# Optimization experiments

Hardware: AMD Instinct MI355X
Metric: run time of the kernel (lower is better)

Reference implementation:

```python
import jax, jax.numpy as jnp
import numpy as np

N_IN, N_LAT, LEN_T, N_SHIFT = 128, 21, 51, 50
N_HID, BATCH = 4, 2048


def identity_init(n_rows, n_cols):
    A = np.zeros((n_rows, n_cols), np.float32)
    if n_rows >= n_cols:
        k = n_rows - n_cols + 1
        for c in range(n_cols):
            A[c:c + k, c] = 1.0 / k
    else:
        k = n_cols - n_rows + 1
        for r in range(n_rows):
            A[r, r:r + k] = 1.0 / k
    return jnp.asarray(A)


def setup_inputs() -> dict:
    key = jax.random.key(0)
    ks = jax.random.split(key, 8)
    s = 0.05
    return {
        'inputs': jax.random.normal(ks[0], (BATCH, LEN_T, N_IN), dtype=jnp.float32),
        'enc_W': jax.random.normal(ks[1], (N_HID, N_IN, N_IN), dtype=jnp.float32) * s,
        'enc_b': jnp.zeros((N_HID, N_IN), jnp.float32),
        'enc_Wout': jax.random.normal(ks[2], (N_IN, N_IN), dtype=jnp.float32) * s,
        'enc_bout': jnp.zeros((N_IN,), jnp.float32),
        'dec_W': jax.random.normal(ks[3], (N_HID, N_IN, N_IN), dtype=jnp.float32) * s,
        'dec_b': jnp.zeros((N_HID, N_IN), jnp.float32),
        'dec_Wout': jax.random.normal(ks[4], (N_IN, N_IN), dtype=jnp.float32) * s,
        'dec_bout': jnp.zeros((N_IN,), jnp.float32),
        'W_enc_inner': identity_init(N_IN, N_LAT),
        'L': jnp.eye(N_LAT, dtype=jnp.float32),
        'W_dec_inner': identity_init(N_LAT, N_IN),
    }


def res_block(x, Ws, bs, Wout, bout):
    # DenseResBlock: ReLU hidden dense stack + linear output + identity skip
    h = x
    for i in range(Ws.shape[0]):
        h = jax.nn.relu(h @ Ws[i] + bs[i])
    return h @ Wout + bout + x


def reference(inputs, enc_W, enc_b, enc_Wout, enc_bout,
              dec_W, dec_b, dec_Wout, dec_bout,
              W_enc_inner, L, W_dec_inner):
    B = inputs.shape[0]
    len_pred = LEN_T - N_SHIFT  # = 1

    # ---- autoencoder branch (all timesteps flattened into rows) ----
    auto_in = inputs.reshape(-1, N_IN)                       # [B*T, n_in]
    part_enc = res_block(auto_in, enc_W, enc_b, enc_Wout, enc_bout)
    full_enc = part_enc @ W_enc_inner                        # [B*T, n_lat]
    part_dec = full_enc @ W_dec_inner                        # [B*T, n_in]
    autoencoder_output = res_block(part_dec, dec_W, dec_b, dec_Wout, dec_bout)
    autoencoder_output = autoencoder_output.reshape(B, LEN_T, N_IN)
    outer_auto_output = res_block(part_enc, dec_W, dec_b, dec_Wout, dec_bout)
    outer_auto_output = outer_auto_output.reshape(B, LEN_T, N_IN)

    # ---- prediction branch: recurrent application of Koopman operator L ----
    pred_in = inputs[:, :len_pred, :].reshape(-1, N_IN)      # [B*len_pred, n_in]
    cur = res_block(pred_in, enc_W, enc_b, enc_Wout, enc_bout) @ W_enc_inner

    def step(cur_enc, _):
        adv = cur_enc @ L                                    # [B*len_pred, n_lat]
        dec = res_block(adv @ W_dec_inner, dec_W, dec_b, dec_Wout, dec_bout)
        return adv, dec

    _, preds = jax.lax.scan(step, cur, None, length=N_SHIFT)  # [S, B*lp, n_in]
    preds = preds.reshape(N_SHIFT, B, len_pred, N_IN)
    predictions = preds.transpose(1, 0, 2, 3).reshape(B, N_SHIFT * len_pred, N_IN)

    return autoencoder_output, outer_auto_output, predictions
```

## Files before the change

kernel.cpp:

```cpp
#include <hip/hip_runtime.h>
#include <stdint.h>


typedef _Float16 h8 __attribute__((ext_vector_type(8)));
typedef _Float16 h4 __attribute__((ext_vector_type(4)));
typedef float    f4 __attribute__((ext_vector_type(4)));

#define ROWS_AUTO 104448
#define NT64      1632
#define NUNITS    2432

#define WT_ENCW      0
#define WT_ENCWOUT   (4*16384)
#define WT_DECW      (5*16384)
#define WT_DECWOUT   (9*16384)
#define WT_COMB      (10*16384)

#define MFULL_OFF_B 0x60000
#define ACH_OFF_B   0x200000
#define PE_OFF_B    0x220000
#define PET0_OFF_B  0x1C00000

#define H0 0
#define H1 16384
#define H2 32768
#define H3 49152
#define LDSE (49152 + 2560)
#define LDSD (65536 + 2560)

#define hsw(rl, c) ((rl)*256 + ((((c)) ^ ((rl) & 7)) << 4))

#define PIN(B) asm volatile("" : "+v"(B[0]), "+v"(B[1]), "+v"(B[2]), "+v"(B[3]), \
                                 "+v"(B[4]), "+v"(B[5]), "+v"(B[6]), "+v"(B[7]))

__device__ __forceinline__ f4 mfma16(h8 a, h8 b, f4 c) {
  return __builtin_amdgcn_mfma_f32_16x16x32_f16(a, b, c, 0, 0, 0);
}
__device__ __forceinline__ h8 cvt8(f4 a, f4 b) {
  h8 r;
  r[0]=(_Float16)a[0]; r[1]=(_Float16)a[1]; r[2]=(_Float16)a[2]; r[3]=(_Float16)a[3];
  r[4]=(_Float16)b[0]; r[5]=(_Float16)b[1]; r[6]=(_Float16)b[2]; r[7]=(_Float16)b[3];
  return r;
}
__device__ __forceinline__ void loadW(h8 B[8], const _Float16* gW, int nbase, int r15, int hi) {
#pragma unroll
  for (int nt = 0; nt < 2; ++nt)
#pragma unroll
    for (int ks = 0; ks < 4; ++ks)
      B[nt*4+ks] = *(const h8*)(gW + (size_t)(nbase + nt*16 + r15)*128 + ks*32 + hi*8);
}

__device__ __forceinline__ void mmF4s(const char* sm, int hb, const h8 B[8],
                                      f4 acc[4][2], int r15, int hi) {
#pragma unroll
  for (int rt = 0; rt < 4; ++rt) { acc[rt][0] = (f4){0,0,0,0}; acc[rt][1] = (f4){0,0,0,0}; }
#pragma unroll
  for (int ks = 0; ks < 4; ++ks) {
    int c = ks*4 + hi;
    h8 a[4];
#pragma unroll
    for (int rt = 0; rt < 4; ++rt) a[rt] = *(const h8*)(sm + hb + hsw(rt*16 + r15, c));
#pragma unroll
    for (int rt = 0; rt < 4; ++rt) {
      acc[rt][0] = mfma16(B[ks],   a[rt], acc[rt][0]);
      acc[rt][1] = mfma16(B[4+ks], a[rt], acc[rt][1]);
    }
  }
}

__device__ __forceinline__ void hw4s(char* sm, int hb, int wbase, const f4 acc[4][2],
                                     const float* bl, int bo, int r15, int hi) {
  f4 bb0 = *(const f4*)(bl + bo + wbase + hi*4);
  f4 bb1 = *(const f4*)(bl + bo + wbase + 16 + hi*4);
  int bo2 = (hi & 1) * 8;
#pragma unroll
  for (int nt = 0; nt < 2; ++nt) {
    int c = ((wbase + nt*16) >> 3) + (hi >> 1);
    f4 bb = nt ? bb1 : bb0;
#pragma unroll
    for (int rt = 0; rt < 4; ++rt) {
      int row = rt*16 + r15;
      h4 p;
#pragma unroll
      for (int d = 0; d < 4; ++d) p[d] = (_Float16)fmaxf(acc[rt][nt][d] + bb[d], 0.f);
      *(h4*)(sm + hb + row*256 + ((c ^ (row & 7)) << 4) + bo2) = p;
    }
  }
}
__device__ __forceinline__ void hw4r(char* sm, int hb, int wbase, const f4 acc[4][2],
                                     int r15, int hi) {
  int bo2 = (hi & 1) * 8;
#pragma unroll
  for (int nt = 0; nt < 2; ++nt) {
    int c = ((wbase + nt*16) >> 3) + (hi >> 1);
#pragma unroll
    for (int rt = 0; rt < 4; ++rt) {
      int row = rt*16 + r15;
      h4 p;
#pragma unroll
      for (int d = 0; d < 4; ++d) p[d] = (_Float16)acc[rt][nt][d];
      *(h4*)(sm + hb + row*256 + ((c ^ (row & 7)) << 4) + bo2) = p;
    }
  }
}

__device__ __forceinline__ void epi_direct(const char* sm, int hskip, int wbase,
                                           const f4 acc[4][2], const float* bl,
                                           float* dst, int rstride, int r15, int hi) {
  f4 bb0 = *(const f4*)(bl + 512 + wbase + hi*4);
  f4 bb1 = *(const f4*)(bl + 512 + wbase + 16 + hi*4);
  int bo2 = (hi & 1) * 8;
#pragma unroll
  for (int nt = 0; nt < 2; ++nt) {
    int c = ((wbase + nt*16) >> 3) + (hi >> 1);
    int n0 = wbase + nt*16 + hi*4;
    f4 bb = nt ? bb1 : bb0;
#pragma unroll
    for (int rt = 0; rt < 4; ++rt) {
      int row = rt*16 + r15;
      h4 sk = *(const h4*)(sm + hskip + row*256 + ((c ^ (row & 7)) << 4) + bo2);
      f4 v;
#pragma unroll
      for (int d = 0; d < 4; ++d) v[d] = acc[rt][nt][d] + bb[d] + (float)sk[d];
      *(f4*)(dst + (size_t)row*rstride + n0) = v;
    }
  }
}

#define LAYD(HIN, HOUT, BW, BO) do {                                 \
    mmF4s(sm, HIN, BW, acc, r15, hi);                                \
    hw4s(sm, HOUT, wbase, acc, bl, BO, r15, hi);                     \
    __syncthreads();                                                 \
  } while (0)


__global__ __launch_bounds__(512) void k_prep(
    const float* __restrict__ encW, const float* __restrict__ encWout,
    const float* __restrict__ decW, const float* __restrict__ decWout,
    const float* __restrict__ L,
    _Float16* __restrict__ wt, float* __restrict__ ach) {
  __shared__ float chA[441], chB[441];
  int m = blockIdx.y, tid = threadIdx.x;
  if (m == 10) {
    if (blockIdx.x != 0) return;
    if (tid < 441) chA[tid] = L[tid];
    __syncthreads();
    for (int s = 0; s < 50; ++s) {
      if (tid < 441) ach[s*441 + tid] = chA[tid];
      if (s == 49) break;
      if (tid < 441) {
        int i = tid / 21, j = tid % 21; float a = 0.f;
        for (int k = 0; k < 21; ++k) a += chA[i*21 + k] * L[k*21 + j];
        chB[tid] = a;
      }
      __syncthreads();
      if (tid < 441) chA[tid] = chB[tid];
      __syncthreads();
    }
    return;
  }
  int idx = blockIdx.x*512 + tid;
  if (idx >= 16384) return;
  const float* src; _Float16* dst;
  if (m < 4)       { src = encW + m*16384;     dst = wt + WT_ENCW + m*16384; }
  else if (m == 4) { src = encWout;            dst = wt + WT_ENCWOUT; }
  else if (m < 9)  { src = decW + (m-5)*16384; dst = wt + WT_DECW + (m-5)*16384; }
  else             { src = decWout;            dst = wt + WT_DECWOUT; }
  int n = idx >> 7, k = idx & 127;
  dst[idx] = (_Float16)src[k*128 + n];
}

__global__ __launch_bounds__(512) void k_aux(
    const float* __restrict__ ach, const float* __restrict__ wencI,
    const float* __restrict__ wdecI,
    _Float16* __restrict__ mfull, _Float16* __restrict__ wt) {
  __shared__ float T1[2688];
  __shared__ float sa[441];
  int s = blockIdx.x, t = threadIdx.x;
  if (s < 50) {
    if (t < 441) sa[t] = ach[s*441 + t];
    __syncthreads();
    for (int idx = t; idx < 2688; idx += 512) {
      int k = idx / 21, j = idx % 21;
      float a = 0.f;
      for (int u = 0; u < 21; ++u) a += wencI[k*21 + u] * sa[u*21 + j];
      T1[idx] = a;
    }
  } else {
    for (int idx = t; idx < 2688; idx += 512) T1[idx] = wencI[idx];
  }
  __syncthreads();
  _Float16* dst = (s < 50) ? (mfull + (size_t)s*16384) : (wt + WT_COMB);
  for (int idx = t; idx < 16384; idx += 512) {
    int n = idx >> 7, k = idx & 127;
    float a = 0.f;
    for (int j = 0; j < 21; ++j) a += T1[k*21 + j] * wdecI[j*128 + n];
    dst[idx] = (_Float16)a;
  }
}


__global__ __launch_bounds__(256, 2) void k_enc(
    const float* __restrict__ x, const _Float16* __restrict__ wt,
    const float* __restrict__ enc_b, const float* __restrict__ enc_bout,
    _Float16* __restrict__ pe_ws, _Float16* __restrict__ pet0) {
  __shared__ char sm[LDSE];
  float* bl = (float*)(sm + 49152);
  int tid = threadIdx.x, lane = tid & 63;
  int r15 = lane & 15, hi = lane >> 4;
  int wbase = (tid >> 6) * 32;
  h8 B0[8], B1[8], B2[8], B3[8], B4[8];
  loadW(B0, wt + WT_ENCW,           wbase, r15, hi);
  loadW(B1, wt + WT_ENCW + 16384,   wbase, r15, hi);
  loadW(B2, wt + WT_ENCW + 2*16384, wbase, r15, hi);
  loadW(B3, wt + WT_ENCW + 3*16384, wbase, r15, hi);
  loadW(B4, wt + WT_ENCWOUT,        wbase, r15, hi);
  PIN(B0); PIN(B1); PIN(B2); PIN(B3); PIN(B4);
  bl[tid] = enc_b[tid]; bl[256 + tid] = enc_b[256 + tid];
  if (tid < 128) bl[512 + tid] = enc_bout[tid];
  f4 acc[4][2];

  for (int t = blockIdx.x; t < NT64; t += gridDim.x) {
    size_t rb = (size_t)t * 64;
#pragma unroll
    for (int i = 0; i < 4; ++i) {
      int idx = i*256 + tid, rl = idx >> 4, c = idx & 15;
      const float* s = x + (rb + rl)*128 + c*8;
      f4 v0 = *(const f4*)s, v1 = *(const f4*)(s + 4);
      *(h8*)(sm + H0 + hsw(rl, c)) = cvt8(v0, v1);
    }
    __syncthreads();
    LAYD(H0, H1, B0, 0); LAYD(H1, H2, B1, 128);
    LAYD(H2, H1, B2, 256); LAYD(H1, H2, B3, 384);
    mmF4s(sm, H2, B4, acc, r15, hi);
    {
      f4 bb0 = *(const f4*)(bl + 512 + wbase + hi*4);
      f4 bb1 = *(const f4*)(bl + 512 + wbase + 16 + hi*4);
      int bo2 = (hi & 1) * 8;
#pragma unroll
      for (int nt = 0; nt < 2; ++nt) {
        int c = ((wbase + nt*16) >> 3) + (hi >> 1);
        f4 bb = nt ? bb1 : bb0;
#pragma unroll
        for (int rt = 0; rt < 4; ++rt) {
          int row = rt*16 + r15;
          int soff = H0 + row*256 + ((c ^ (row & 7)) << 4) + bo2;
          h4 sk = *(const h4*)(sm + soff);
          h4 p;
#pragma unroll
          for (int d = 0; d < 4; ++d) p[d] = (_Float16)(acc[rt][nt][d] + bb[d] + (float)sk[d]);
          *(h4*)(sm + soff) = p;
        }
      }
    }
    __syncthreads();
    {
      char* g = (char*)(pe_ws) + (size_t)t*16384;
#pragma unroll
      for (int i = 0; i < 4; ++i) {
        int idx = i*256 + tid, off = idx*16;
        f4 v = *(const f4*)(sm + H0 + off);
        *(f4*)(g + off) = v;
        int rl = idx >> 4, slot = idx & 15;
        size_t rg = rb + (size_t)rl;
        if (rg % 51u == 0u) {
          int c = slot ^ (rl & 7);
          *(f4*)((char*)pet0 + (rg/51u)*256 + c*16) = v;
        }
      }
    }
    __syncthreads();
  }
}


__global__ __launch_bounds__(256, 2) void k_decpred(
    const _Float16* __restrict__ wt, const _Float16* __restrict__ pe_ws,
    const _Float16* __restrict__ pet0, const _Float16* __restrict__ mfull,
    const float* __restrict__ dec_b, const float* __restrict__ dec_bout,
    float* __restrict__ out1, float* __restrict__ out2, float* __restrict__ out3) {
  __shared__ char sm[LDSD];
  float* bl = (float*)(sm + 65536);
  int tid = threadIdx.x, lane = tid & 63;
  int r15 = lane & 15, hi = lane >> 4;
  int wbase = (tid >> 6) * 32;
  h8 B0[8], B1[8], B2[8], B3[8], B4[8];
  loadW(B0, wt + WT_DECW,           wbase, r15, hi);
  loadW(B1, wt + WT_DECW + 16384,   wbase, r15, hi);
  loadW(B2, wt + WT_DECW + 2*16384, wbase, r15, hi);
  loadW(B3, wt + WT_DECW + 3*16384, wbase, r15, hi);
  loadW(B4, wt + WT_DECWOUT,        wbase, r15, hi);
  PIN(B0); PIN(B1); PIN(B2); PIN(B3); PIN(B4);
  bl[tid] = dec_b[tid]; bl[256 + tid] = dec_b[256 + tid];
  if (tid < 128) bl[512 + tid] = dec_bout[tid];
  f4 acc[4][2];

  for (int u = blockIdx.x; u < NUNITS; u += gridDim.x) {
    __syncthreads();
    if (u < NT64) {
      const char* src = (const char*)pe_ws + (size_t)u*16384;
#pragma unroll
      for (int i = 0; i < 4; ++i) {
        int off = (i*256 + tid)*16;
        *(f4*)(sm + H0 + off) = *(const f4*)(src + off);
      }
      __syncthreads();
      LAYD(H0, H1, B0, 0); LAYD(H1, H2, B1, 128);
      LAYD(H2, H1, B2, 256); LAYD(H1, H2, B3, 384);
      mmF4s(sm, H2, B4, acc, r15, hi);
      epi_direct(sm, H0, wbase, acc, bl,
                 out2 + (size_t)u*64*128, 128, r15, hi);
      {
        h8 Bc[8];
        loadW(Bc, wt + WT_COMB, wbase, r15, hi);
        mmF4s(sm, H0, Bc, acc, r15, hi);
      }
      hw4r(sm, H3, wbase, acc, r15, hi);
      __syncthreads();
      LAYD(H3, H0, B0, 0); LAYD(H0, H1, B1, 128);
      LAYD(H1, H0, B2, 256); LAYD(H0, H1, B3, 384);
      mmF4s(sm, H1, B4, acc, r15, hi);
      epi_direct(sm, H3, wbase, acc, bl,
                 out1 + (size_t)u*64*128, 128, r15, hi);
    } else {
      int p = u - NT64, rtile = p / 25, chunk = p % 25;
#pragma unroll
      for (int i = 0; i < 4; ++i) {
        int idx = i*256 + tid, rl = idx >> 4, c = idx & 15;
        f4 v = *(const f4*)((const char*)pet0 + (size_t)(rtile*64 + rl)*256 + c*16);
        *(f4*)(sm + H0 + hsw(rl, c)) = v;
      }
      __syncthreads();
      for (int s = chunk*2; s < chunk*2 + 2; ++s) {
        {
          h8 Bm[8];
          loadW(Bm, mfull + (size_t)s*16384, wbase, r15, hi);
          mmF4s(sm, H0, Bm, acc, r15, hi);
        }
        hw4r(sm, H1, wbase, acc, r15, hi);
        __syncthreads();
        LAYD(H1, H2, B0, 0); LAYD(H2, H3, B1, 128);
        LAYD(H3, H2, B2, 256); LAYD(H2, H3, B3, 384);
        mmF4s(sm, H3, B4, acc, r15, hi);
        epi_direct(sm, H1, wbase, acc, bl,
                   out3 + ((size_t)rtile*64*50 + s)*128, 50*128, r15, hi);
        __syncthreads();
      }
    }
  }
}


extern "C" void kernel_launch(void* const* d_in, const int* in_sizes, int n_in,
                              void* d_out, int out_size, void* d_ws, size_t ws_size,
                              hipStream_t stream) {
  const float* x        = (const float*)d_in[0];
  const float* encW     = (const float*)d_in[1];
  const float* enc_b    = (const float*)d_in[2];
  const float* encWout  = (const float*)d_in[3];
  const float* enc_bout = (const float*)d_in[4];
  const float* decW     = (const float*)d_in[5];
  const float* dec_b    = (const float*)d_in[6];
  const float* decWout  = (const float*)d_in[7];
  const float* dec_bout = (const float*)d_in[8];
  const float* wencI    = (const float*)d_in[9];
  const float* L        = (const float*)d_in[10];
  const float* wdecI    = (const float*)d_in[11];

  char* ws = (char*)d_ws;
  _Float16* wt    = (_Float16*)ws;
  _Float16* mfull = (_Float16*)(ws + MFULL_OFF_B);
  float*    ach   = (float*)(ws + ACH_OFF_B);
  _Float16* pe_ws = (_Float16*)(ws + PE_OFF_B);
  _Float16* pet0  = (_Float16*)(ws + PET0_OFF_B);

  float* out1 = (float*)d_out;
  float* out2 = out1 + (size_t)ROWS_AUTO*128;
  float* out3 = out2 + (size_t)ROWS_AUTO*128;

  hipLaunchKernelGGL(k_prep, dim3(32, 11), dim3(512), 0, stream,
                     encW, encWout, decW, decWout, L, wt, ach);
  hipLaunchKernelGGL(k_aux, dim3(51), dim3(512), 0, stream,
                     ach, wencI, wdecI, mfull, wt);
  hipLaunchKernelGGL(k_enc, dim3(512), dim3(256), 0, stream,
                     x, wt, enc_b, enc_bout, pe_ws, pet0);
  hipLaunchKernelGGL(k_decpred, dim3(512), dim3(256), 0, stream,
                     wt, pe_ws, pet0, mfull, dec_b, dec_bout, out1, out2, out3);
}
```

Before: 198.2 us.

## Fuse encoder and decoder/prediction kernels with atomic work queue and per-tile flags

Merges the encoder and decoder/prediction kernels into one persistent kernel. Blocks pull tiles from global atomic counters, and per-tile release/acquire flags let decoder work start as soon as its encoded tile is ready. This removes a kernel launch boundary and the tail idle time between the two phases. The combined weight is also held in registers instead of being reloaded per tile, which raises register pressure. The spin-waits rely on all 512 blocks being co-resident and add atomic traffic.

```diff
diff --git a/kernel.cpp b/kernel.cpp
--- a/kernel.cpp
+++ b/kernel.cpp
@@ -20,13 +20,13 @@
 #define ACH_OFF_B   0x200000
 #define PE_OFF_B    0x220000
 #define PET0_OFF_B  0x1C00000
+#define CTRL_OFF_B  0x1D00000
 
 #define H0 0
 #define H1 16384
 #define H2 32768
 #define H3 49152
-#define LDSE (49152 + 2560)
-#define LDSD (65536 + 2560)
+#define LDSF (65536 + 2560 + 16)
 
 #define hsw(rl, c) ((rl)*256 + ((((c)) ^ ((rl) & 7)) << 4))
 
@@ -200,16 +200,24 @@
 }
 
 
-__global__ __launch_bounds__(256, 2) void k_enc(
+__global__ __launch_bounds__(256, 2) void k_fused(
     const float* __restrict__ x, const _Float16* __restrict__ wt,
+    const _Float16* __restrict__ mfull,
     const float* __restrict__ enc_b, const float* __restrict__ enc_bout,
-    _Float16* __restrict__ pe_ws, _Float16* __restrict__ pet0) {
-  __shared__ char sm[LDSE];
-  float* bl = (float*)(sm + 49152);
+    const float* __restrict__ dec_b, const float* __restrict__ dec_bout,
+    float* __restrict__ out1, float* __restrict__ out2, float* __restrict__ out3,
+    _Float16* __restrict__ pe_ws, _Float16* __restrict__ pet0,
+    int* __restrict__ ctrl) {
+  __shared__ char sm[LDSF];
+  float* bl = (float*)(sm + 65536);
+  int* tk = (int*)(sm + 65536 + 2560);
+  int* flags = ctrl + 4;
   int tid = threadIdx.x, lane = tid & 63;
   int r15 = lane & 15, hi = lane >> 4;
   int wbase = (tid >> 6) * 32;
   h8 B0[8], B1[8], B2[8], B3[8], B4[8];
+  f4 acc[4][2];
+
   loadW(B0, wt + WT_ENCW,           wbase, r15, hi);
   loadW(B1, wt + WT_ENCW + 16384,   wbase, r15, hi);
   loadW(B2, wt + WT_ENCW + 2*16384, wbase, r15, hi);
@@ -218,9 +226,14 @@
   PIN(B0); PIN(B1); PIN(B2); PIN(B3); PIN(B4);
   bl[tid] = enc_b[tid]; bl[256 + tid] = enc_b[256 + tid];
   if (tid < 128) bl[512 + tid] = enc_bout[tid];
-  f4 acc[4][2];
-
-  for (int t = blockIdx.x; t < NT64; t += gridDim.x) {
+
+  for (;;) {
+    __syncthreads();
+    if (tid == 0) *tk = __hip_atomic_fetch_add(&ctrl[0], 1, __ATOMIC_RELAXED,
+                                               __HIP_MEMORY_SCOPE_AGENT);
+    __syncthreads();
+    int t = *tk;
+    if (t >= NT64) break;
     size_t rb = (size_t)t * 64;
 #pragma unroll
     for (int i = 0; i < 4; ++i) {
@@ -270,34 +283,36 @@
       }
     }
     __syncthreads();
-  }
-}
-
-
-__global__ __launch_bounds__(256, 2) void k_decpred(
-    const _Float16* __restrict__ wt, const _Float16* __restrict__ pe_ws,
-    const _Float16* __restrict__ pet0, const _Float16* __restrict__ mfull,
-    const float* __restrict__ dec_b, const float* __restrict__ dec_bout,
-    float* __restrict__ out1, float* __restrict__ out2, float* __restrict__ out3) {
-  __shared__ char sm[LDSD];
-  float* bl = (float*)(sm + 65536);
-  int tid = threadIdx.x, lane = tid & 63;
-  int r15 = lane & 15, hi = lane >> 4;
-  int wbase = (tid >> 6) * 32;
-  h8 B0[8], B1[8], B2[8], B3[8], B4[8];
+    if (tid == 0) {
+      __hip_atomic_store(&flags[t], 1, __ATOMIC_RELEASE, __HIP_MEMORY_SCOPE_AGENT);
+      __hip_atomic_fetch_add(&ctrl[2], 1, __ATOMIC_RELEASE, __HIP_MEMORY_SCOPE_AGENT);
+    }
+  }
+
+  h8 B5[8];
   loadW(B0, wt + WT_DECW,           wbase, r15, hi);
   loadW(B1, wt + WT_DECW + 16384,   wbase, r15, hi);
   loadW(B2, wt + WT_DECW + 2*16384, wbase, r15, hi);
   loadW(B3, wt + WT_DECW + 3*16384, wbase, r15, hi);
   loadW(B4, wt + WT_DECWOUT,        wbase, r15, hi);
-  PIN(B0); PIN(B1); PIN(B2); PIN(B3); PIN(B4);
+  loadW(B5, wt + WT_COMB,           wbase, r15, hi);
+  PIN(B0); PIN(B1); PIN(B2); PIN(B3); PIN(B4); PIN(B5);
+  __syncthreads();
   bl[tid] = dec_b[tid]; bl[256 + tid] = dec_b[256 + tid];
   if (tid < 128) bl[512 + tid] = dec_bout[tid];
-  f4 acc[4][2];
-
-  for (int u = blockIdx.x; u < NUNITS; u += gridDim.x) {
-    __syncthreads();
+
+  for (;;) {
+    __syncthreads();
+    if (tid == 0) *tk = __hip_atomic_fetch_add(&ctrl[1], 1, __ATOMIC_RELAXED,
+                                               __HIP_MEMORY_SCOPE_AGENT);
+    __syncthreads();
+    int u = *tk;
+    if (u >= NUNITS) break;
     if (u < NT64) {
+      if (tid == 0)
+        while (__hip_atomic_load(&flags[u], __ATOMIC_ACQUIRE, __HIP_MEMORY_SCOPE_AGENT) == 0)
+          __builtin_amdgcn_s_sleep(2);
+      __syncthreads();
       const char* src = (const char*)pe_ws + (size_t)u*16384;
 #pragma unroll
       for (int i = 0; i < 4; ++i) {
@@ -310,11 +325,7 @@
       mmF4s(sm, H2, B4, acc, r15, hi);
       epi_direct(sm, H0, wbase, acc, bl,
                  out2 + (size_t)u*64*128, 128, r15, hi);
-      {
-        h8 Bc[8];
-        loadW(Bc, wt + WT_COMB, wbase, r15, hi);
-        mmF4s(sm, H0, Bc, acc, r15, hi);
-      }
+      mmF4s(sm, H0, B5, acc, r15, hi);
       hw4r(sm, H3, wbase, acc, r15, hi);
       __syncthreads();
       LAYD(H3, H0, B0, 0); LAYD(H0, H1, B1, 128);
@@ -323,6 +334,10 @@
       epi_direct(sm, H3, wbase, acc, bl,
                  out1 + (size_t)u*64*128, 128, r15, hi);
     } else {
+      if (tid == 0)
+        while (__hip_atomic_load(&ctrl[2], __ATOMIC_ACQUIRE, __HIP_MEMORY_SCOPE_AGENT) < NT64)
+          __builtin_amdgcn_s_sleep(2);
+      __syncthreads();
       int p = u - NT64, rtile = p / 25, chunk = p % 25;
 #pragma unroll
       for (int i = 0; i < 4; ++i) {
@@ -373,17 +388,18 @@
   float*    ach   = (float*)(ws + ACH_OFF_B);
   _Float16* pe_ws = (_Float16*)(ws + PE_OFF_B);
   _Float16* pet0  = (_Float16*)(ws + PET0_OFF_B);
+  int*      ctrl  = (int*)(ws + CTRL_OFF_B);
 
   float* out1 = (float*)d_out;
   float* out2 = out1 + (size_t)ROWS_AUTO*128;
   float* out3 = out2 + (size_t)ROWS_AUTO*128;
 
+  hipMemsetAsync(ctrl, 0, sizeof(int)*(4 + NT64), stream);
   hipLaunchKernelGGL(k_prep, dim3(32, 11), dim3(512), 0, stream,
                      encW, encWout, decW, decWout, L, wt, ach);
   hipLaunchKernelGGL(k_aux, dim3(51), dim3(512), 0, stream,
                      ach, wencI, wdecI, mfull, wt);
-  hipLaunchKernelGGL(k_enc, dim3(512), dim3(256), 0, stream,
-                     x, wt, enc_b, enc_bout, pe_ws, pet0);
-  hipLaunchKernelGGL(k_decpred, dim3(512), dim3(256), 0, stream,
-                     wt, pe_ws, pet0, mfull, dec_b, dec_bout, out1, out2, out3);
-}
+  hipLaunchKernelGGL(k_fused, dim3(512), dim3(256), 0, stream,
+                     x, wt, mfull, enc_b, enc_bout, dec_b, dec_bout,
+                     out1, out2, out3, pe_ws, pet0, ctrl);
+}
```

New measurement: 333.9 us. 1.68x slower.

## Prefetch next tile's inputs into registers and raise MFMA wave priority

Applied to the files above, without the earlier changes.

In both the encoder and decoder persistent loops, the global loads for the next tile are issued into registers while the current tile's MFMA layers run, then written to LDS at the start of the next iteration. This hides global-memory latency behind compute. Separately, s_setprio raises wave priority around the MFMA inner loop so matrix work is scheduled ahead of other waves. The cost is extra live VGPRs (32 or 16 floats per thread) on top of the 40 pinned weight vectors, which could cause spills or lower occupancy.

```diff
diff --git a/kernel.cpp b/kernel.cpp
--- a/kernel.cpp
+++ b/kernel.cpp
@@ -54,6 +54,7 @@
                                       f4 acc[4][2], int r15, int hi) {
 #pragma unroll
   for (int rt = 0; rt < 4; ++rt) { acc[rt][0] = (f4){0,0,0,0}; acc[rt][1] = (f4){0,0,0,0}; }
+  __builtin_amdgcn_s_setprio(1);
 #pragma unroll
   for (int ks = 0; ks < 4; ++ks) {
     int c = ks*4 + hi;
@@ -66,6 +67,7 @@
       acc[rt][1] = mfma16(B[4+ks], a[rt], acc[rt][1]);
     }
   }
+  __builtin_amdgcn_s_setprio(0);
 }
 
 __device__ __forceinline__ void hw4s(char* sm, int hb, int wbase, const f4 acc[4][2],
@@ -219,20 +221,42 @@
   bl[tid] = enc_b[tid]; bl[256 + tid] = enc_b[256 + tid];
   if (tid < 128) bl[512 + tid] = enc_bout[tid];
   f4 acc[4][2];
+  f4 pfx[8];
+  bool pfv = false;
 
   for (int t = blockIdx.x; t < NT64; t += gridDim.x) {
     size_t rb = (size_t)t * 64;
-#pragma unroll
-    for (int i = 0; i < 4; ++i) {
-      int idx = i*256 + tid, rl = idx >> 4, c = idx & 15;
-      const float* s = x + (rb + rl)*128 + c*8;
-      f4 v0 = *(const f4*)s, v1 = *(const f4*)(s + 4);
-      *(h8*)(sm + H0 + hsw(rl, c)) = cvt8(v0, v1);
+    if (pfv) {
+#pragma unroll
+      for (int i = 0; i < 4; ++i) {
+        int idx = i*256 + tid, rl = idx >> 4, c = idx & 15;
+        *(h8*)(sm + H0 + hsw(rl, c)) = cvt8(pfx[2*i], pfx[2*i+1]);
+      }
+    } else {
+#pragma unroll
+      for (int i = 0; i < 4; ++i) {
+        int idx = i*256 + tid, rl = idx >> 4, c = idx & 15;
+        const float* s = x + (rb + rl)*128 + c*8;
+        f4 v0 = *(const f4*)s, v1 = *(const f4*)(s + 4);
+        *(h8*)(sm + H0 + hsw(rl, c)) = cvt8(v0, v1);
+      }
     }
     __syncthreads();
     LAYD(H0, H1, B0, 0); LAYD(H1, H2, B1, 128);
     LAYD(H2, H1, B2, 256); LAYD(H1, H2, B3, 384);
     mmF4s(sm, H2, B4, acc, r15, hi);
+    {
+      int tn = t + (int)gridDim.x;
+      pfv = (tn < NT64);
+      if (pfv) {
+#pragma unroll
+        for (int i = 0; i < 4; ++i) {
+          int idx = i*256 + tid, rl = idx >> 4, c = idx & 15;
+          const float* s = x + ((size_t)tn*64 + rl)*128 + c*8;
+          pfx[2*i] = *(const f4*)s; pfx[2*i+1] = *(const f4*)(s + 4);
+        }
+      }
+    }
     {
       f4 bb0 = *(const f4*)(bl + 512 + wbase + hi*4);
       f4 bb1 = *(const f4*)(bl + 512 + wbase + 16 + hi*4);
@@ -294,17 +318,34 @@
   bl[tid] = dec_b[tid]; bl[256 + tid] = dec_b[256 + tid];
   if (tid < 128) bl[512 + tid] = dec_bout[tid];
   f4 acc[4][2];
+  f4 pf[4];
+  bool pfv = false;
 
   for (int u = blockIdx.x; u < NUNITS; u += gridDim.x) {
     __syncthreads();
     if (u < NT64) {
-      const char* src = (const char*)pe_ws + (size_t)u*16384;
-#pragma unroll
-      for (int i = 0; i < 4; ++i) {
-        int off = (i*256 + tid)*16;
-        *(f4*)(sm + H0 + off) = *(const f4*)(src + off);
+      if (pfv) {
+#pragma unroll
+        for (int i = 0; i < 4; ++i)
+          *(f4*)(sm + H0 + (i*256 + tid)*16) = pf[i];
+      } else {
+        const char* src = (const char*)pe_ws + (size_t)u*16384;
+#pragma unroll
+        for (int i = 0; i < 4; ++i) {
+          int off = (i*256 + tid)*16;
+          *(f4*)(sm + H0 + off) = *(const f4*)(src + off);
+        }
       }
       __syncthreads();
+      {
+        int un = u + (int)gridDim.x;
+        pfv = (un < NT64);
+        if (pfv) {
+          const char* s2 = (const char*)pe_ws + (size_t)un*16384;
+#pragma unroll
+          for (int i = 0; i < 4; ++i) pf[i] = *(const f4*)(s2 + (i*256 + tid)*16);
+        }
+      }
       LAYD(H0, H1, B0, 0); LAYD(H1, H2, B1, 128);
       LAYD(H2, H1, B2, 256); LAYD(H1, H2, B3, 384);
       mmF4s(sm, H2, B4, acc, r15, hi);
@@ -323,6 +364,7 @@
       epi_direct(sm, H3, wbase, acc, bl,
                  out1 + (size_t)u*64*128, 128, r15, hi);
     } else {
+      pfv = false;
       int p = u - NT64, rtile = p / 25, chunk = p % 25;
 #pragma unroll
       for (int i = 0; i < 4; ++i) {
```

Result: slower. 227.2 us (+14.6%).
